# Kernel tuning notes

Hardware: AMD Instinct MI355X
Metric: run time of the kernel (lower is better)

## Reference

```python
import jax, jax.numpy as jnp
import numpy as np

B, N, NE = 16, 96, 256
ATOM, EDIM, HID, LAT, HEADS = 128, 16, 128, 128, 4
HD = LAT // HEADS
RBF, CUT, ZEMB, MAXZ = 16, 5.0, 32, 100
MUL0_IN, MUL1_IN = 64, 32      # irreps_node = 64x0e + 32x1o (dim 160)
MUL0_OUT, MUL1_OUT = 32, 16    # out irreps  = 32x0e + 16x1o (dim 80)
NODE_DIM = MUL0_IN + 3 * MUL1_IN
OUT_DIM = MUL0_OUT + 3 * MUL1_OUT
E_ATT = 1024
WNUM = MUL0_IN*MUL0_OUT + MUL0_IN*MUL1_OUT + MUL1_IN*MUL1_OUT + MUL1_IN*MUL0_OUT  # 4608


def _mlp3(x, w1, b1, w2, b2, w3, b3):
    x = jax.nn.silu(x @ w1 + b1)
    x = jax.nn.silu(x @ w2 + b2)
    return x @ w3 + b3


def setup_inputs() -> dict:
    key = jax.random.key(0)
    ks = jax.random.split(key, 40)
    s = 0.05  # scale params so deep MLP activations stay numerically sane
    d = {}
    d['h'] = jax.random.normal(ks[0], (B, N, ATOM), jnp.float32)
    d['h_full'] = jax.random.normal(ks[1], (B, N, NODE_DIM), jnp.float32)
    d['e_feat'] = jax.random.normal(ks[2], (NE, EDIM), jnp.float32)
    d['att_dist'] = jax.random.uniform(ks[3], (E_ATT,), jnp.float32)
    d['att_vec'] = jax.random.normal(ks[4], (E_ATT, 3), jnp.float32)
    d['z_emb_table'] = jax.random.normal(ks[5], (MAXZ + 1, ZEMB), jnp.float32) * s
    d['rw1'] = jax.random.normal(ks[6], (ZEMB + 1 + RBF, HID), jnp.float32) * s
    d['rb1'] = jnp.zeros((HID,), jnp.float32)
    d['rw2'] = jax.random.normal(ks[7], (HID, WNUM), jnp.float32) * s
    d['rb2'] = jnp.zeros((WNUM,), jnp.float32)
    d['ew1'] = jax.random.normal(ks[8], (EDIM, HID), jnp.float32) * s
    d['eb1'] = jnp.zeros((HID,), jnp.float32)
    d['ew2'] = jax.random.normal(ks[9], (HID, MUL0_OUT + MUL1_OUT), jnp.float32) * s
    d['eb2'] = jnp.zeros((MUL0_OUT + MUL1_OUT,), jnp.float32)
    d['qw1'] = jax.random.normal(ks[10], (ATOM + EDIM, HID), jnp.float32) * s
    d['qb1'] = jnp.zeros((HID,), jnp.float32)
    d['qw2'] = jax.random.normal(ks[11], (HID, HID), jnp.float32) * s
    d['qb2'] = jnp.zeros((HID,), jnp.float32)
    d['qw3'] = jax.random.normal(ks[12], (HID, LAT), jnp.float32) * s
    d['qb3'] = jnp.zeros((LAT,), jnp.float32)
    d['kw1'] = jax.random.normal(ks[13], (ATOM + ZEMB + 1 + RBF, HID), jnp.float32) * s
    d['kb1'] = jnp.zeros((HID,), jnp.float32)
    d['kw2'] = jax.random.normal(ks[14], (HID, HID), jnp.float32) * s
    d['kb2'] = jnp.zeros((HID,), jnp.float32)
    d['kw3'] = jax.random.normal(ks[15], (HID, LAT), jnp.float32) * s
    d['kb3'] = jnp.zeros((LAT,), jnp.float32)
    d['ow1'] = jax.random.normal(ks[16], (MUL0_OUT + MUL1_OUT, HID), jnp.float32) * s
    d['ob1'] = jnp.zeros((HID,), jnp.float32)
    d['ow2'] = jax.random.normal(ks[17], (HID, HID), jnp.float32) * s
    d['ob2'] = jnp.zeros((HID,), jnp.float32)
    d['ow3'] = jax.random.normal(ks[18], (HID, LAT), jnp.float32) * s
    d['ob3'] = jnp.zeros((LAT,), jnp.float32)
    d['z'] = jax.random.randint(ks[19], (B, N), 0, MAXZ)
    d['mask'] = jnp.ones((B, N), bool)
    d['absorber_index'] = jax.random.randint(ks[20], (B,), 0, N)
    d['att_dst'] = jnp.arange(E_ATT)  # unique flat indices into B*N
    return d


def reference(h, h_full, e_feat, att_dist, att_vec, z_emb_table,
              rw1, rb1, rw2, rb2, ew1, eb1, ew2, eb2,
              qw1, qb1, qw2, qb2, qw3, qb3,
              kw1, kb1, kw2, kb2, kw3, kb3,
              ow1, ob1, ow2, ob2, ow3, ob3,
              z, mask, absorber_index, att_dst):
    Bz, Na, Hd = h.shape
    F = Bz * Na
    nE = e_feat.shape[0]
    # scatter edge data into flat (B*N) atom slots
    am_flat = jnp.zeros((F,), bool).at[att_dst].set(True)
    d_flat = jnp.zeros((F,), h.dtype).at[att_dst].set(att_dist)
    v_flat = jnp.zeros((F, 3), h.dtype).at[att_dst].set(att_vec)
    att_mask = am_flat.reshape(Bz, Na) & mask
    # spherical harmonics (lmax=1, component normalization): Y0 = 1, Y1 = sqrt(3)*unit_vec
    un = v_flat / jnp.maximum(jnp.linalg.norm(v_flat, axis=-1, keepdims=True), 1e-8)
    y1 = jnp.sqrt(3.0) * un
    # Gaussian RBF on absorber->atom distance
    mu = jnp.linspace(0.0, CUT, RBF)
    delta = CUT / (RBF - 1)
    rbf = jnp.exp(-(d_flat[:, None] - mu) ** 2 / (2.0 * delta * delta))  # (F, RBF)
    zr = z_emb_table[z]                      # (B, N, ZEMB)
    zr_flat = zr.reshape(F, -1)
    is_abs = jnp.zeros((Bz, Na), h.dtype).at[jnp.arange(Bz), absorber_index].set(1.0)
    # radial MLP -> per-edge tensor-product weights
    w_in = jnp.concatenate([zr_flat, is_abs.reshape(F, 1), rbf], -1)
    tpw = jax.nn.silu(w_in @ rw1 + rb1) @ rw2 + rb2  # (F, WNUM)
    s1 = MUL0_IN * MUL0_OUT
    s2 = s1 + MUL0_IN * MUL1_OUT
    s3 = s2 + MUL1_IN * MUL1_OUT
    w00 = tpw[:, :s1].reshape(F, MUL0_IN, MUL0_OUT)   # 0e x 0e -> 0e
    w01 = tpw[:, s1:s2].reshape(F, MUL0_IN, MUL1_OUT) # 0e x 1o -> 1o
    w10 = tpw[:, s2:s3].reshape(F, MUL1_IN, MUL1_OUT) # 1o x 0e -> 1o
    w11 = tpw[:, s3:].reshape(F, MUL1_IN, MUL0_OUT)   # 1o x 1o -> 0e
    hf = h_full.reshape(F, -1)
    x0 = hf[:, :MUL0_IN]
    x1 = hf[:, MUL0_IN:].reshape(F, MUL1_IN, 3)
    alpha = 1.0 / jnp.sqrt(jnp.float32(MUL0_IN + MUL1_IN))  # path fan-in normalization
    c = 1.0 / jnp.sqrt(3.0)                                  # wigner-3j coeff for l=1 couplings
    out0 = alpha * (jnp.einsum('fi,fio->fo', x0, w00)
                    + c * jnp.einsum('fim,fm,fio->fo', x1, y1, w11))
    out1 = alpha * c * (jnp.einsum('fi,fm,fio->fom', x0, y1, w01)
                        + jnp.einsum('fim,fio->fom', x1, w10))
    v_irrep = jnp.concatenate([out0, out1.reshape(F, 3 * MUL1_OUT)], -1)  # (F, OUT_DIM)
    # cosine cutoff envelope + edge mask
    env = jnp.where(d_flat < CUT, 0.5 * (jnp.cos(jnp.pi * d_flat / CUT) + 1.0), 0.0)
    v_irrep = v_irrep * (am_flat.astype(h.dtype) * env)[:, None]
    # energy-conditioned per-irrep-channel modulation
    gates = jax.nn.silu(e_feat @ ew1 + eb1) @ ew2 + eb2  # (nE, 48)
    g_exp = jnp.concatenate([gates[:, :MUL0_OUT],
                             jnp.repeat(gates[:, MUL0_OUT:], 3, axis=-1)], -1)  # (nE, OUT_DIM)
    v_mod = (v_irrep[:, None, :] * g_exp[None]).reshape(Bz, Na, nE, OUT_DIM)
    # invariant multi-head scoring
    h_abs = h[jnp.arange(Bz), absorber_index]  # (B, H)
    q_in = jnp.concatenate([jnp.broadcast_to(h_abs[:, None], (Bz, nE, Hd)),
                            jnp.broadcast_to(e_feat[None], (Bz, nE, EDIM))], -1)
    q = _mlp3(q_in, qw1, qb1, qw2, qb2, qw3, qb3)  # (B, nE, LAT)
    atom_static = jnp.concatenate([h, zr, is_abs[..., None], rbf.reshape(Bz, Na, RBF)], -1)
    k = _mlp3(atom_static, kw1, kb1, kw2, kb2, kw3, kb3)  # (B, N, LAT)
    qh = q.reshape(Bz, nE, HEADS, HD)
    kh = k.reshape(Bz, Na, HEADS, HD)
    scores = (jnp.einsum('behd,bnhd->benh', qh, kh) * (HD ** -0.5)).mean(-1)  # (B, nE, N)
    m = att_mask[:, None, :]
    scores = jnp.where(m, scores, -1e9)
    attn = jax.nn.softmax(scores, axis=2) * m.astype(h.dtype)
    attn = attn / jnp.maximum(attn.sum(2, keepdims=True), 1e-8)
    out_irrep = jnp.einsum('ben,bnec->bec', attn, v_mod)  # (B, nE, OUT_DIM)
    # invariants: scalars + vector norms
    scal = out_irrep[..., :MUL0_OUT]
    vec = out_irrep[..., MUL0_OUT:].reshape(Bz, nE, MUL1_OUT, 3)
    inv = jnp.concatenate([scal, jnp.sqrt(jnp.sum(vec * vec, -1) + 1e-12)], -1)
    return _mlp3(inv, ow1, ob1, ow2, ob2, ow3, ob3)  # (B, nE, LAT)
```

## Files before the change

### kernel.cpp

```cpp
#include <hip/hip_runtime.h>
#include <hip/hip_fp16.h>
#include <math.h>

#define BB 16
#define NN 96
#define NE 256
#define FF (BB*NN)
#define ATOM 128
#define EDIM 16
#define HID 128
#define LAT 128
#define RBFN 16
#define CUTOFF 5.0f
#define ZEMB 32
#define E_ATT 1024
#define M0I 64
#define M1I 32
#define M0O 32
#define M1O 16
#define NODE_DIM 160
#define OUT_DIM 80
#define INVD 48
#define WNUM 4608
#define SEG1 2048
#define SEG2 3072
#define SEG3 3584

#define S1_EDGE 256
#define S1_Q    512
#define S1_GATE 16
#define S1_TRANS 144
#define STAGE1_BLKS 929

#define TP_BLKS 192
#define SCORE_BLKS 128
#define K2_BLKS (TP_BLKS + SCORE_BLKS)

#define CSTR 1544

typedef _Float16 half8_t __attribute__((ext_vector_type(8)));
typedef float float4v __attribute__((ext_vector_type(4)));

__device__ __forceinline__ float silu_f(float x) { return x / (1.0f + expf(-x)); }

__global__ __launch_bounds__(256) void k_stage1(
    const float* __restrict__ h, const float* __restrict__ z_emb, const int* __restrict__ z,
    const int* __restrict__ absorber, const float* __restrict__ e_feat,
    const int* __restrict__ att_dst, const float* __restrict__ att_dist,
    const float* __restrict__ att_vec,
    const float* __restrict__ rw1, const float* __restrict__ rb1,
    const float* __restrict__ kw1, const float* __restrict__ kb1,
    const float* __restrict__ kw2, const float* __restrict__ kb2,
    const float* __restrict__ kw3, const float* __restrict__ kb3,
    const float* __restrict__ qw1, const float* __restrict__ qb1,
    const float* __restrict__ qw2, const float* __restrict__ qb2,
    const float* __restrict__ qw3, const float* __restrict__ qb3,
    const float* __restrict__ ew1, const float* __restrict__ eb1,
    const float* __restrict__ ew2, const float* __restrict__ eb2,
    const float* __restrict__ rw2,
    __half* __restrict__ hiddenH, float* __restrict__ kmatw,
    float* __restrict__ qmat, float* __restrict__ gexp,
    __half* __restrict__ rw2T,
    int* __restrict__ inv, float* __restrict__ y1E, float* __restrict__ envE)
{
    __shared__ float smem[3488];
    int blk = blockIdx.x;
    int t = threadIdx.x;

    if (blk < S1_EDGE) {
        float (*sin1)[184] = (float(*)[184])smem;
        float (*l1S)[128]  = (float(*)[128])(smem + 736);
        float (*l2S)[128]  = (float(*)[128])(smem + 736 + 512);
        int w = t >> 6;
        int c = t & 63;
        int e = blk*4 + w;
        int f = att_dst[e];
        int b = f / NN, nn = f - b*NN;
        float d = att_dist[e];
        {
            float2 hv = *(const float2*)&h[f*ATOM + 2*c];
            sin1[w][2*c] = hv.x; sin1[w][2*c + 1] = hv.y;
        }
        if (c < ZEMB) sin1[w][ATOM + c] = z_emb[z[f]*ZEMB + c];
        if (c >= 32 && c < 48) {
            int j = c - 32;
            const float delta = CUTOFF / (RBFN - 1);
            float diff = d - j*delta;
            sin1[w][ATOM + ZEMB + 1 + j] = expf(-diff*diff / (2.0f*delta*delta));
        }
        if (c == 48) sin1[w][ATOM + ZEMB] = (absorber[b] == nn) ? 1.0f : 0.0f;
        __builtin_amdgcn_wave_barrier();
        int c2 = 2*c;
        {
            float2 a0 = *(const float2*)&rb1[c2];
            float2 a1 = make_float2(0.f, 0.f);
            #pragma unroll 8
            for (int i = 0; i < 48; i += 2) {
                float x0v = sin1[w][ATOM + i], x1v = sin1[w][ATOM + i + 1];
                float2 w0 = *(const float2*)&rw1[i*HID + c2];
                float2 w1 = *(const float2*)&rw1[(i+1)*HID + c2];
                a0.x += x0v*w0.x; a0.y += x0v*w0.y;
                a1.x += x1v*w1.x; a1.y += x1v*w1.y;
            }
            {
                float x0v = sin1[w][ATOM + 48];
                float2 w0 = *(const float2*)&rw1[48*HID + c2];
                a0.x += x0v*w0.x; a0.y += x0v*w0.y;
            }
            *(__half2*)&hiddenH[e*HID + c2] =
                __floats2half2_rn(silu_f(a0.x + a1.x), silu_f(a0.y + a1.y));
        }
        {
            float2 a0 = *(const float2*)&kb1[c2];
            float2 a1 = make_float2(0.f, 0.f);
            #pragma unroll 16
            for (int i = 0; i < 176; i += 2) {
                float x0v = sin1[w][i], x1v = sin1[w][i + 1];
                float2 w0 = *(const float2*)&kw1[i*HID + c2];
                float2 w1 = *(const float2*)&kw1[(i+1)*HID + c2];
                a0.x += x0v*w0.x; a0.y += x0v*w0.y;
                a1.x += x1v*w1.x; a1.y += x1v*w1.y;
            }
            {
                float x0v = sin1[w][176];
                float2 w0 = *(const float2*)&kw1[176*HID + c2];
                a0.x += x0v*w0.x; a0.y += x0v*w0.y;
            }
            l1S[w][c2] = silu_f(a0.x + a1.x); l1S[w][c2+1] = silu_f(a0.y + a1.y);
        }
        __builtin_amdgcn_wave_barrier();
        {
            float2 a0 = *(const float2*)&kb2[c2];
            float2 a1 = make_float2(0.f, 0.f);
            #pragma unroll 16
            for (int i = 0; i < HID; i += 2) {
                float x0v = l1S[w][i], x1v = l1S[w][i + 1];
                float2 w0 = *(const float2*)&kw2[i*HID + c2];
                float2 w1 = *(const float2*)&kw2[(i+1)*HID + c2];
                a0.x += x0v*w0.x; a0.y += x0v*w0.y;
                a1.x += x1v*w1.x; a1.y += x1v*w1.y;
            }
            l2S[w][c2] = silu_f(a0.x + a1.x); l2S[w][c2+1] = silu_f(a0.y + a1.y);
        }
        __builtin_amdgcn_wave_barrier();
        {
            float2 a0 = *(const float2*)&kb3[c2];
            float2 a1 = make_float2(0.f, 0.f);
            #pragma unroll 16
            for (int i = 0; i < HID; i += 2) {
                float x0v = l2S[w][i], x1v = l2S[w][i + 1];
                float2 w0 = *(const float2*)&kw3[i*HID + c2];
                float2 w1 = *(const float2*)&kw3[(i+1)*HID + c2];
                a0.x += x0v*w0.x; a0.y += x0v*w0.y;
                a1.x += x1v*w1.x; a1.y += x1v*w1.y;
            }
            float2 o; o.x = a0.x + a1.x; o.y = a0.y + a1.y;
            *(float2*)&kmatw[f*HID + c2] = o;
        }
    } else if (blk < S1_EDGE + S1_Q) {
        float* hA          = smem;
        float (*ef)[16]    = (float(*)[16])(smem + 128);
        float (*part)[128] = (float(*)[128])(smem + 256);
        float* l1S         = smem + 1280;
        float* l2S         = smem + 2304;
        int idx = blk - S1_EDGE;
        int r0 = idx * 8;
        int b  = r0 >> 8;
        int e8 = r0 & 255;
        if (t < 32) *(float4*)&hA[t*4] = *(const float4*)&h[(b*NN + absorber[b])*ATOM + t*4];
        if (t >= 128 && t < 256) { int e = (t - 128) >> 4, j = t & 15; ef[e][j] = e_feat[(e8 + e)*EDIM + j]; }
        __syncthreads();
        int r = t >> 5, c0 = (t & 31)*4;
        {
            float4 a0 = make_float4(0,0,0,0);
            int k0 = r*16;
            #pragma unroll
            for (int k = 0; k < 16; k++) {
                float hv = hA[k0 + k];
                float4 w0 = *(const float4*)&qw1[(k0 + k)*HID + c0];
                a0.x += hv*w0.x; a0.y += hv*w0.y; a0.z += hv*w0.z; a0.w += hv*w0.w;
            }
            *(float4*)&part[r][c0] = a0;
        }
        __syncthreads();
        {
            float4 s = *(const float4*)&qb1[c0];
            #pragma unroll
            for (int g = 0; g < 8; g++) {
                float4 pg = *(const float4*)&part[g][c0];
                s.x += pg.x; s.y += pg.y; s.z += pg.z; s.w += pg.w;
            }
            #pragma unroll
            for (int j = 0; j < 16; j++) {
                float a = ef[r][j];
                float4 w0 = *(const float4*)&qw1[(ATOM + j)*HID + c0];
                s.x += a*w0.x; s.y += a*w0.y; s.z += a*w0.z; s.w += a*w0.w;
            }
            l1S[r*128 + c0]   = silu_f(s.x); l1S[r*128 + c0+1] = silu_f(s.y);
            l1S[r*128 + c0+2] = silu_f(s.z); l1S[r*128 + c0+3] = silu_f(s.w);
        }
        __syncthreads();
        {
            float4 a0 = *(const float4*)&qb2[c0];
            float4 a1 = make_float4(0,0,0,0);
            #pragma unroll 8
            for (int i = 0; i < HID; i += 2) {
                float x0v = l1S[r*128 + i], x1v = l1S[r*128 + i+1];
                float4 w0 = *(const float4*)&qw2[i*HID + c0];
                float4 w1 = *(const float4*)&qw2[(i+1)*HID + c0];
                a0.x += x0v*w0.x; a0.y += x0v*w0.y; a0.z += x0v*w0.z; a0.w += x0v*w0.w;
                a1.x += x1v*w1.x; a1.y += x1v*w1.y; a1.z += x1v*w1.z; a1.w += x1v*w1.w;
            }
            l2S[r*128 + c0]   = silu_f(a0.x + a1.x); l2S[r*128 + c0+1] = silu_f(a0.y + a1.y);
            l2S[r*128 + c0+2] = silu_f(a0.z + a1.z); l2S[r*128 + c0+3] = silu_f(a0.w + a1.w);
        }
        __syncthreads();
        {
            float4 a0 = *(const float4*)&qb3[c0];
            float4 a1 = make_float4(0,0,0,0);
            #pragma unroll 8
            for (int i = 0; i < HID; i += 2) {
                float x0v = l2S[r*128 + i], x1v = l2S[r*128 + i+1];
                float4 w0 = *(const float4*)&qw3[i*HID + c0];
                float4 w1 = *(const float4*)&qw3[(i+1)*HID + c0];
                a0.x += x0v*w0.x; a0.y += x0v*w0.y; a0.z += x0v*w0.z; a0.w += x0v*w0.w;
                a1.x += x1v*w1.x; a1.y += x1v*w1.y; a1.z += x1v*w1.z; a1.w += x1v*w1.w;
            }
            float4 o;
            o.x = a0.x + a1.x; o.y = a0.y + a1.y; o.z = a0.z + a1.z; o.w = a0.w + a1.w;
            *(float4*)&qmat[(r0 + r)*LAT + c0] = o;
        }
    } else if (blk < S1_EDGE + S1_Q + S1_GATE) {
        float (*ef)[16]   = (float(*)[16])smem;
        float (*l1g)[128] = (float(*)[128])(smem + 256);
        float (*gg)[48]   = (float(*)[48])(smem + 256 + 2048);
        int e0 = (blk - S1_EDGE - S1_Q) * 16;
        { int e = t >> 4, i = t & 15; ef[e][i] = e_feat[(e0 + e)*EDIM + i]; }
        __syncthreads();
        int r = t >> 4, c0 = (t & 15)*8;
        {
            float4 a0 = *(const float4*)&eb1[c0];
            float4 a1 = *(const float4*)&eb1[c0 + 4];
            #pragma unroll
            for (int i = 0; i < EDIM; i++) {
                float a = ef[r][i];
                float4 w0 = *(const float4*)&ew1[i*HID + c0];
                float4 w1 = *(const float4*)&ew1[i*HID + c0 + 4];
                a0.x += a*w0.x; a0.y += a*w0.y; a0.z += a*w0.z; a0.w += a*w0.w;
                a1.x += a*w1.x; a1.y += a*w1.y; a1.z += a*w1.z; a1.w += a*w1.w;
            }
            l1g[r][c0]   = silu_f(a0.x); l1g[r][c0+1] = silu_f(a0.y);
            l1g[r][c0+2] = silu_f(a0.z); l1g[r][c0+3] = silu_f(a0.w);
            l1g[r][c0+4] = silu_f(a1.x); l1g[r][c0+5] = silu_f(a1.y);
            l1g[r][c0+6] = silu_f(a1.z); l1g[r][c0+7] = silu_f(a1.w);
        }
        __syncthreads();
        for (int u = t; u < 16*48; u += 256) {
            int e = u / 48, j = u - 48*(u/48);
            float acc = eb2[j];
            #pragma unroll 4
            for (int i = 0; i < HID; i++) acc += l1g[e][i]*ew2[i*48 + j];
            gg[e][j] = acc;
        }
        __syncthreads();
        for (int u = t; u < 16*80; u += 256) {
            int e = u / 80, cc = u - 80*(u/80);
            gexp[(e0 + e)*OUT_DIM + cc] = (cc < M0O) ? gg[e][cc] : gg[e][M0O + (cc - M0O)/3];
        }
    } else if (blk < S1_EDGE + S1_Q + S1_GATE + S1_TRANS) {
        __half* lds = (__half*)smem;
        int tb = blk - (S1_EDGE + S1_Q + S1_GATE);
        int nt = tb % 72, kt = tb / 72;
        int n0 = nt*64, k0 = kt*64;
        for (int p = 0; p < 16; p++) {
            int idx = t + 256*p;
            int kk = idx >> 6, nn = idx & 63;
            lds[nn*66 + kk] = __float2half(rw2[(k0+kk)*WNUM + n0+nn]);
        }
        __syncthreads();
        for (int p = 0; p < 16; p++) {
            int idx = t + 256*p;
            int nn = idx >> 6, kk = idx & 63;
            rw2T[(n0+nn)*HID + k0+kk] = lds[nn*66 + kk];
        }
    } else {
        for (int p = 0; p < 6; p++) inv[t + 256*p] = -1;
        for (int p = 0; p < 4; p++) {
            int e = t + 256*p;
            float d = att_dist[e];
            envE[e] = (d < CUTOFF) ? 0.5f*(cosf(3.14159265358979323846f*d/CUTOFF) + 1.0f) : 0.0f;
            float vx = att_vec[3*e], vy = att_vec[3*e+1], vz = att_vec[3*e+2];
            float nrm = sqrtf(vx*vx + vy*vy + vz*vz);
            float is = 1.0f / fmaxf(nrm, 1e-8f);
            const float s3 = 1.7320508075688772f;
            y1E[3*e]   = s3*vx*is;
            y1E[3*e+1] = s3*vy*is;
            y1E[3*e+2] = s3*vz*is;
        }
        __syncthreads();
        for (int p = 0; p < 4; p++) { int e = t + 256*p; inv[att_dst[e]] = e; }
    }
}

__global__ __launch_bounds__(256) void k_fuse(
    const __half* __restrict__ hiddenH, const __half* __restrict__ rw2T,
    const float* __restrict__ rb2,
    const float* __restrict__ qmat, const float* __restrict__ kmat,
    const int* __restrict__ inv, const int* __restrict__ att_dst,
    const float* __restrict__ h_full,
    const float* __restrict__ envE, const float* __restrict__ y1E,
    float* __restrict__ virr, float* __restrict__ scoresW)
{
    __shared__ __align__(16) char smemraw[62208];
    float* smem = (float*)smemraw;
    int blk = blockIdx.x;
    int t = threadIdx.x;
    if (blk < TP_BLKS) {
        __half* cS   = (__half*)smemraw;
        float* fbase = (float*)(smemraw + 49408);
        float* x0f   = fbase;
        float* x1f   = fbase + 1024;
        float* xyf   = fbase + 2560;
        float* y1f   = fbase + 3072;
        float* envf  = fbase + 3136;
        int*   fI    = (int*)(fbase + 3152);
        int cls  = blk % 3;
        int tile = blk / 3;
        int e0 = tile * 16;
        if (t < 16) {
            int e = e0 + t;
            fI[t] = att_dst[e];
            envf[t] = envE[e];
            y1f[t*4]   = y1E[3*e];
            y1f[t*4+1] = y1E[3*e+1];
            y1f[t*4+2] = y1E[3*e+2];
        }
        __syncthreads();
        for (int p = 0; p < 10; p++) {
            int idx = t + 256*p;
            int edge = idx / 160, j = idx - 160*edge;
            float v = h_full[fI[edge]*NODE_DIM + j];
            if (j < M0I) x0f[edge*64 + j] = v;
            else         x1f[edge*96 + (j - M0I)] = v;
        }
        __syncthreads();
        for (int p = 0; p < 2; p++) {
            int idx = t + 256*p;
            int edge = idx >> 5, i = idx & 31;
            xyf[edge*32 + i] = x1f[edge*96 + 3*i]*y1f[edge*4]
                             + x1f[edge*96 + 3*i+1]*y1f[edge*4+1]
                             + x1f[edge*96 + 3*i+2]*y1f[edge*4+2];
        }

        int wv = t >> 6;
        int lane = t & 63;
        int mrow = lane & 15, quad = lane >> 4;
        const _Float16* hp = (const _Float16*)hiddenH + (e0 + mrow)*HID + quad*8;
        half8_t af[4];
        #pragma unroll
        for (int kc = 0; kc < 4; kc++) af[kc] = *(const half8_t*)(hp + kc*32);

        int clsAdd = (cls == 1) ? 1 : 0;
        #pragma unroll 4
        for (int jj = 0; jj < 24; jj++) {
            int j = wv*24 + jj;
            int ntg = (cls == 2) ? (128 + j)
                                 : (2*j + clsAdd + ((j >= 64) ? 96 : 0));
            const _Float16* bp = (const _Float16*)rw2T + (ntg*16 + mrow)*HID + quad*8;
            float4v acc = {0.f, 0.f, 0.f, 0.f};
            #pragma unroll
            for (int kc = 0; kc < 4; kc++) {
                half8_t bf = *(const half8_t*)(bp + kc*32);
                acc = __builtin_amdgcn_mfma_f32_16x16x32_f16(af[kc], bf, acc, 0, 0, 0);
            }
            float bias = rb2[ntg*16 + mrow];
            #pragma unroll
            for (int r = 0; r < 4; r++)
                cS[(quad*4 + r)*CSTR + j*16 + mrow] = __float2half(acc[r] + bias);
        }
        __syncthreads();

        int edge = t >> 4, o = t & 15;
        const __half* cRow = cS + edge*CSTR + o;
        const float alpha = 0.10206207261596575f;
        const float ccf   = 0.5773502691896258f;
        int f = fI[edge];
        float env = envf[edge];
        if (cls < 2) {
            float t00 = 0.f, t11 = 0.f;
            #pragma unroll 8
            for (int j = 0; j < 64; j++)
                t00 += x0f[edge*64 + j]*__half2float(cRow[j*16]);
            #pragma unroll 8
            for (int j = 64; j < 96; j++)
                t11 += xyf[edge*32 + (j - 64)]*__half2float(cRow[j*16]);
            virr[f*OUT_DIM + cls*16 + o] = alpha*(t00 + ccf*t11)*env;
        } else {
            float t01 = 0.f, tm0 = 0.f, tm1 = 0.f, tm2 = 0.f;
            #pragma unroll 8
            for (int j = 0; j < 64; j++)
                t01 += x0f[edge*64 + j]*__half2float(cRow[j*16]);
            #pragma unroll 8
            for (int j = 64; j < 96; j++) {
                int i = j - 64;
                float C = __half2float(cRow[j*16]);
                tm0 += x1f[edge*96 + 3*i]*C;
                tm1 += x1f[edge*96 + 3*i+1]*C;
                tm2 += x1f[edge*96 + 3*i+2]*C;
            }
            float y0 = y1f[edge*4], y1v = y1f[edge*4+1], y2 = y1f[edge*4+2];
            virr[f*OUT_DIM + M0O + 3*o]     = alpha*ccf*(t01*y0 + tm0)*env;
            virr[f*OUT_DIM + M0O + 3*o + 1] = alpha*ccf*(t01*y1v + tm1)*env;
            virr[f*OUT_DIM + M0O + 3*o + 2] = alpha*ccf*(t01*y2 + tm2)*env;
        }
    } else {
        int u = blk - TP_BLKS;
        int b  = u >> 3;
        int e0 = (u & 7) * 32;
        float (*Qs)[132] = (float(*)[132])smem;
        float (*Kt)[132] = (float(*)[132])(smem + 32*132);
        float* mS = smem + 2*32*132;
        for (int p = 0; p < 4; p++) {
            int idx = t + 256*p; int e = idx >> 5, i4 = idx & 31;
            *(float4*)&Qs[e][i4*4] = *(const float4*)&qmat[(b*NE + e0 + e)*LAT + i4*4];
        }
        if (t < NN) mS[t] = ((unsigned)inv[b*NN + t] < E_ATT) ? 1.0f : 0.0f;
        int te = t >> 5, tn = t & 31;
        float acc[4][3] = {};
        for (int nt = 0; nt < 3; nt++) {
            __syncthreads();
            for (int p = 0; p < 4; p++) {
                int idx = t + 256*p; int n = idx >> 5, i4 = idx & 31;
                *(float4*)&Kt[n][i4*4] = *(const float4*)&kmat[(b*NN + nt*32 + n)*LAT + i4*4];
            }
            __syncthreads();
            for (int i = 0; i < LAT; i++) {
                float bv = Kt[tn][i];
                acc[0][nt] += Qs[te*4 + 0][i]*bv;
                acc[1][nt] += Qs[te*4 + 1][i]*bv;
                acc[2][nt] += Qs[te*4 + 2][i]*bv;
                acc[3][nt] += Qs[te*4 + 3][i]*bv;
            }
        }
        const float scale = 0.04419417382415922f;
        #pragma unroll
        for (int j = 0; j < 4; j++)
            #pragma unroll
            for (int jj = 0; jj < 3; jj++) {
                int n = tn + 32*jj;
                float s = (mS[n] != 0.f) ? acc[j][jj]*scale : -1e9f;
                scoresW[((b*NE) + e0 + te*4 + j)*NN + n] = s;
            }
    }
}

__global__ __launch_bounds__(256) void k_attf(
    const float* __restrict__ scoresW, const int* __restrict__ inv,
    const float* __restrict__ virr, const float* __restrict__ gexp,
    const float* __restrict__ ow1, const float* __restrict__ ob1,
    const float* __restrict__ ow2, const float* __restrict__ ob2,
    const float* __restrict__ ow3, const float* __restrict__ ob3,
    float* __restrict__ out)
{
    int b  = blockIdx.x >> 5;
    int e0 = (blockIdx.x & 31) * 8;
    int t = threadIdx.x;
    __shared__ float aS[8][100];
    __shared__ float gS[8][84];
    __shared__ float ocS[8][84];
    __shared__ float mS[NN];
    __shared__ float inS[8][INVD];
    __shared__ float l1S[8][HID];
    __shared__ float l2S[8][HID];

    for (int p = 0; p < 3; p++) {
        int idx = t + 256*p;
        int el = idx / NN, n = idx - NN*(idx/NN);
        aS[el][n] = scoresW[((b*NE) + e0 + el)*NN + n];
    }
    if (t < 160) {
        int el = t / 20, c4 = t - 20*(t/20);
        *(float4*)&gS[el][c4*4] = *(const float4*)&gexp[(e0 + el)*OUT_DIM + c4*4];
    }
    if (t < NN) mS[t] = ((unsigned)inv[b*NN + t] < E_ATT) ? 1.0f : 0.0f;
    __syncthreads();

    {
        int el = t >> 5;
        int ng = t & 31;
        float s0 = aS[el][ng], s1 = aS[el][ng + 32], s2 = aS[el][ng + 64];
        float m0 = mS[ng], m1 = mS[ng + 32], m2 = mS[ng + 64];
        float mx = fmaxf(s0, fmaxf(s1, s2));
        #pragma unroll
        for (int off = 1; off < 32; off <<= 1) mx = fmaxf(mx, __shfl_xor(mx, off));
        float e0v = expf(s0 - mx), e1v = expf(s1 - mx), e2v = expf(s2 - mx);
        float sm = e0v + e1v + e2v;
        #pragma unroll
        for (int off = 1; off < 32; off <<= 1) sm += __shfl_xor(sm, off);
        float r = 1.0f / sm;
        float p0 = m0*e0v*r, p1 = m1*e1v*r, p2 = m2*e2v*r;
        float ss = p0 + p1 + p2;
        #pragma unroll
        for (int off = 1; off < 32; off <<= 1) ss += __shfl_xor(ss, off);
        float is = 1.0f / fmaxf(ss, 1e-8f);
        aS[el][ng]      = p0*is;
        aS[el][ng + 32] = p1*is;
        aS[el][ng + 64] = p2*is;
    }
    __syncthreads();

    if (t < 160) {
        int el = t / 20, c4 = t - 20*(t/20);
        const float* vp = virr + (long)b*NN*OUT_DIM + c4*4;
        float4 acc = make_float4(0,0,0,0);
        #pragma unroll 4
        for (int n = 0; n < NN; n++) {
            float a = aS[el][n];
            float4 v = *(const float4*)&vp[n*OUT_DIM];
            acc.x += a*v.x; acc.y += a*v.y; acc.z += a*v.z; acc.w += a*v.w;
        }
        float4 g = *(float4*)&gS[el][c4*4];
        float4 o; o.x = acc.x*g.x; o.y = acc.y*g.y; o.z = acc.z*g.z; o.w = acc.w*g.w;
        *(float4*)&ocS[el][c4*4] = o;
    }
    __syncthreads();

    for (int u = t; u < 8*INVD; u += 256) {
        int el = u / INVD, j = u - INVD*(u/INVD);
        float val;
        if (j < M0O) val = ocS[el][j];
        else {
            int o = j - M0O;
            float x = ocS[el][M0O + 3*o], y = ocS[el][M0O + 3*o + 1], zz = ocS[el][M0O + 3*o + 2];
            val = sqrtf(x*x + y*y + zz*zz + 1e-12f);
        }
        inS[el][j] = val;
    }
    __syncthreads();

    int r = t >> 5, c0 = (t & 31)*4;
    {
        float4 a0 = *(const float4*)&ob1[c0];
        float4 a1 = make_float4(0,0,0,0);
        #pragma unroll 8
        for (int i = 0; i < INVD; i += 2) {
            float x0v = inS[r][i], x1v = inS[r][i+1];
            float4 w0 = *(const float4*)&ow1[i*HID + c0];
            float4 w1 = *(const float4*)&ow1[(i+1)*HID + c0];
            a0.x += x0v*w0.x; a0.y += x0v*w0.y; a0.z += x0v*w0.z; a0.w += x0v*w0.w;
            a1.x += x1v*w1.x; a1.y += x1v*w1.y; a1.z += x1v*w1.z; a1.w += x1v*w1.w;
        }
        l1S[r][c0]   = silu_f(a0.x + a1.x); l1S[r][c0+1] = silu_f(a0.y + a1.y);
        l1S[r][c0+2] = silu_f(a0.z + a1.z); l1S[r][c0+3] = silu_f(a0.w + a1.w);
    }
    __syncthreads();
    {
        float4 a0 = *(const float4*)&ob2[c0];
        float4 a1 = make_float4(0,0,0,0);
        #pragma unroll 8
        for (int i = 0; i < HID; i += 2) {
            float x0v = l1S[r][i], x1v = l1S[r][i+1];
            float4 w0 = *(const float4*)&ow2[i*HID + c0];
            float4 w1 = *(const float4*)&ow2[(i+1)*HID + c0];
            a0.x += x0v*w0.x; a0.y += x0v*w0.y; a0.z += x0v*w0.z; a0.w += x0v*w0.w;
            a1.x += x1v*w1.x; a1.y += x1v*w1.y; a1.z += x1v*w1.z; a1.w += x1v*w1.w;
        }
        l2S[r][c0]   = silu_f(a0.x + a1.x); l2S[r][c0+1] = silu_f(a0.y + a1.y);
        l2S[r][c0+2] = silu_f(a0.z + a1.z); l2S[r][c0+3] = silu_f(a0.w + a1.w);
    }
// ... 13 lines not shown
        o.x = a0.x + a1.x; o.y = a0.y + a1.y; o.z = a0.z + a1.z; o.w = a0.w + a1.w;
        *(float4*)&out[((b*NE + e0) + r)*LAT + c0] = o;
    }
}

extern "C" void kernel_launch(void* const* d_in, const int* in_sizes, int n_in,
                              void* d_out, int out_size, void* d_ws, size_t ws_size,
                              hipStream_t stream) {
    const float* h        = (const float*)d_in[0];
    const float* h_full   = (const float*)d_in[1];
    const float* e_feat   = (const float*)d_in[2];
    const float* att_dist = (const float*)d_in[3];
    const float* att_vec  = (const float*)d_in[4];
    const float* z_emb    = (const float*)d_in[5];
    const float* rw1 = (const float*)d_in[6];  const float* rb1 = (const float*)d_in[7];
    const float* rw2 = (const float*)d_in[8];  const float* rb2 = (const float*)d_in[9];
    const float* ew1 = (const float*)d_in[10]; const float* eb1 = (const float*)d_in[11];
    const float* ew2 = (const float*)d_in[12]; const float* eb2 = (const float*)d_in[13];
    const float* qw1 = (const float*)d_in[14]; const float* qb1 = (const float*)d_in[15];
    const float* qw2 = (const float*)d_in[16]; const float* qb2 = (const float*)d_in[17];
    const float* qw3 = (const float*)d_in[18]; const float* qb3 = (const float*)d_in[19];
    const float* kw1 = (const float*)d_in[20]; const float* kb1 = (const float*)d_in[21];
    const float* kw2 = (const float*)d_in[22]; const float* kb2 = (const float*)d_in[23];
    const float* kw3 = (const float*)d_in[24]; const float* kb3 = (const float*)d_in[25];
    const float* ow1 = (const float*)d_in[26]; const float* ob1 = (const float*)d_in[27];
    const float* ow2 = (const float*)d_in[28]; const float* ob2 = (const float*)d_in[29];
    const float* ow3 = (const float*)d_in[30]; const float* ob3 = (const float*)d_in[31];
    const int* z        = (const int*)d_in[32];
    const int* absorber = (const int*)d_in[34];
    const int* att_dst  = (const int*)d_in[35];

    float* ws = (float*)d_ws;
    int*   inv     = (int*)ws;
    float* y1E     = ws + 1536;
    float* envE    = ws + 4608;
    float* kmat    = ws + 5632;
    float* qmat    = ws + 202240;
    float* gexp    = ws + 726528;
    float* virr    = ws + 747008;
    float* scoresW = ws + 904704;
    __half* rw2T   = (__half*)(ws + 3657216);
    __half* hiddenH= (__half*)(ws + 3952128);

    float* out = (float*)d_out;

    k_stage1<<<STAGE1_BLKS, 256, 0, stream>>>(h, z_emb, z, absorber, e_feat,
                                              att_dst, att_dist, att_vec,
                                              rw1, rb1, kw1, kb1, kw2, kb2, kw3, kb3,
                                              qw1, qb1, qw2, qb2, qw3, qb3,
                                              ew1, eb1, ew2, eb2, rw2,
                                              hiddenH, kmat, qmat, gexp, rw2T,
                                              inv, y1E, envE);
    k_fuse<<<K2_BLKS, 256, 0, stream>>>(hiddenH, rw2T, rb2, qmat, kmat, inv,
                                        att_dst, h_full, envE, y1E, virr, scoresW);
    k_attf<<<BB*32, 256, 0, stream>>>(scoresW, inv, virr, gexp,
                                      ow1, ob1, ow2, ob2, ow3, ob3, out);
}
```

Before: 226.4 us.

## Merge stages into two kernels, fusing tensor product and scores into neighbors

Removes the middle kernel. The tensor-product blocks now compute the radial hidden layer, envelope and spherical harmonics in place and read rw2 directly, converting it to fp16 per element instead of using a pre-transposed copy. The attention scores move into the final kernel, which recomputes q·k per block instead of reading a scores buffer from global memory. This saves a launch and the intermediate buffers. In exchange, rw2 is loaded with strided, uncoalesced reads, and the edge-MLP blocks switch from wave barriers to full block barriers.

```diff
diff --git a/kernel.cpp b/kernel.cpp
--- a/kernel.cpp
+++ b/kernel.cpp
@@ -22,33 +22,29 @@
 #define OUT_DIM 80
 #define INVD 48
 #define WNUM 4608
-#define SEG1 2048
-#define SEG2 3072
-#define SEG3 3584
-
-#define S1_EDGE 256
-#define S1_Q    512
-#define S1_GATE 16
-#define S1_TRANS 144
-#define STAGE1_BLKS 929
-
-#define TP_BLKS 192
-#define SCORE_BLKS 128
-#define K2_BLKS (TP_BLKS + SCORE_BLKS)
-
-#define CSTR 1544
+
+#define K1_TP 192
+#define K1_EDGE_AT 192
+#define K1_Q_AT 448
+#define K1_GATE_AT 960
+#define K1_PREP_AT 976
+#define K1_BLKS 977
+
+#define CSTR2 520
 
 typedef _Float16 half8_t __attribute__((ext_vector_type(8)));
 typedef float float4v __attribute__((ext_vector_type(4)));
 
 __device__ __forceinline__ float silu_f(float x) { return x / (1.0f + expf(-x)); }
 
-__global__ __launch_bounds__(256) void k_stage1(
-    const float* __restrict__ h, const float* __restrict__ z_emb, const int* __restrict__ z,
+__global__ __launch_bounds__(256) void k1(
+    const float* __restrict__ h, const float* __restrict__ h_full,
+    const float* __restrict__ z_emb, const int* __restrict__ z,
     const int* __restrict__ absorber, const float* __restrict__ e_feat,
     const int* __restrict__ att_dst, const float* __restrict__ att_dist,
     const float* __restrict__ att_vec,
     const float* __restrict__ rw1, const float* __restrict__ rb1,
+    const float* __restrict__ rw2, const float* __restrict__ rb2,
     const float* __restrict__ kw1, const float* __restrict__ kb1,
     const float* __restrict__ kw2, const float* __restrict__ kb2,
     const float* __restrict__ kw3, const float* __restrict__ kb3,
@@ -57,23 +53,186 @@
     const float* __restrict__ qw3, const float* __restrict__ qb3,
     const float* __restrict__ ew1, const float* __restrict__ eb1,
     const float* __restrict__ ew2, const float* __restrict__ eb2,
-    const float* __restrict__ rw2,
-    __half* __restrict__ hiddenH, float* __restrict__ kmatw,
-    float* __restrict__ qmat, float* __restrict__ gexp,
-    __half* __restrict__ rw2T,
-    int* __restrict__ inv, float* __restrict__ y1E, float* __restrict__ envE)
+    float* __restrict__ kmatw, float* __restrict__ qmat,
+    float* __restrict__ gexp, float* __restrict__ virr,
+    int* __restrict__ inv)
 {
-    __shared__ float smem[3488];
+    __shared__ __align__(16) char smemraw[36864];
+    float* smem = (float*)smemraw;
     int blk = blockIdx.x;
     int t = threadIdx.x;
 
-    if (blk < S1_EDGE) {
+    if (blk < K1_TP) {
+        __half* cS    = (__half*)smemraw;
+        float*  fbase = (float*)(smemraw + 16640);
+        float* x0f  = fbase;
+        float* x1f  = fbase + 1024;
+        float* xyf  = fbase + 2560;
+        float* y1f  = fbase + 3072;
+        float* envf = fbase + 3136;
+        float* dS   = fbase + 3152;
+        int*   fI   = (int*)(fbase + 3168);
+        float* winf = fbase + 3184;
+        _Float16* hS = (_Float16*)(smemraw + 32704);
+
+        int cls  = blk % 3;
+        int tile = blk / 3;
+        int e0t = tile * 16;
+        if (t < 16) {
+            int e = e0t + t;
+            int f = att_dst[e];
+            fI[t] = f;
+            float d = att_dist[e];
+            dS[t] = d;
+            envf[t] = (d < CUTOFF) ? 0.5f*(cosf(3.14159265358979323846f*d/CUTOFF) + 1.0f) : 0.0f;
+            float vx = att_vec[3*e], vy = att_vec[3*e+1], vz = att_vec[3*e+2];
+            float nrm = sqrtf(vx*vx + vy*vy + vz*vz);
+            float is = 1.0f / fmaxf(nrm, 1e-8f);
+            const float s3 = 1.7320508075688772f;
+            y1f[t*4]   = s3*vx*is;
+            y1f[t*4+1] = s3*vy*is;
+            y1f[t*4+2] = s3*vz*is;
+        }
+        __syncthreads();
+        for (int u = t; u < 16*49; u += 256) {
+            int e = u / 49, j = u - 49*(u/49);
+            int f = fI[e];
+            float v;
+            if (j < ZEMB) v = z_emb[z[f]*ZEMB + j];
+            else if (j == ZEMB) { int b = f / NN, nn = f - b*NN; v = (absorber[b] == nn) ? 1.0f : 0.0f; }
+            else {
+                int jr = j - 33;
+                const float delta = CUTOFF / (RBFN - 1);
+                float diff = dS[e] - jr*delta;
+                v = expf(-diff*diff / (2.0f*delta*delta));
+            }
+            winf[e*52 + j] = v;
+        }
+        for (int p = 0; p < 10; p++) {
+            int idx = t + 256*p;
+            int edge = idx / 160, j = idx - 160*edge;
+            float v = h_full[fI[edge]*NODE_DIM + j];
+            if (j < M0I) x0f[edge*64 + j] = v;
+            else         x1f[edge*96 + (j - M0I)] = v;
+        }
+        __syncthreads();
+        for (int p = 0; p < 2; p++) {
+            int idx = t + 256*p;
+            int edge = idx >> 5, i = idx & 31;
+            xyf[edge*32 + i] = x1f[edge*96 + 3*i]*y1f[edge*4]
+                             + x1f[edge*96 + 3*i+1]*y1f[edge*4+1]
+                             + x1f[edge*96 + 3*i+2]*y1f[edge*4+2];
+        }
+        {
+            int e = t >> 4;
+            const float* wf = winf + e*52;
+            #pragma unroll
+            for (int p = 0; p < 4; p++) {
+                int c2 = 2*((t & 15) + 16*p);
+                float2 a0 = *(const float2*)&rb1[c2];
+                float2 a1 = make_float2(0.f, 0.f);
+                #pragma unroll 8
+                for (int i = 0; i < 48; i += 2) {
+                    float x0v = wf[i], x1v = wf[i + 1];
+                    float2 w0 = *(const float2*)&rw1[i*HID + c2];
+                    float2 w1 = *(const float2*)&rw1[(i+1)*HID + c2];
+                    a0.x += x0v*w0.x; a0.y += x0v*w0.y;
+                    a1.x += x1v*w1.x; a1.y += x1v*w1.y;
+                }
+                {
+                    float x0v = wf[48];
+                    float2 w0 = *(const float2*)&rw1[48*HID + c2];
+                    a0.x += x0v*w0.x; a0.y += x0v*w0.y;
+                }
+                *(__half2*)&hS[e*128 + c2] =
+                    __floats2half2_rn(silu_f(a0.x + a1.x), silu_f(a0.y + a1.y));
+            }
+        }
+        __syncthreads();
+
+        int wv = t >> 6;
+        int lane = t & 63;
+        int mrow = lane & 15, quad = lane >> 4;
+        half8_t af[4];
+        #pragma unroll
+        for (int kc = 0; kc < 4; kc++)
+            af[kc] = *(const half8_t*)&hS[mrow*128 + quad*8 + kc*32];
+
+        int edge = t >> 4, o = t & 15;
+        float t00 = 0.f, t11 = 0.f;
+        float t01 = 0.f, tm0 = 0.f, tm1 = 0.f, tm2 = 0.f;
+        int clsAdd = (cls == 1) ? 1 : 0;
+
+        for (int g = 0; g < 3; g++) {
+            #pragma unroll
+            for (int jj = 0; jj < 8; jj++) {
+                int jl = wv*8 + jj;
+                int j = g*32 + jl;
+                int ntg = (cls == 2) ? (128 + j)
+                                     : (2*j + clsAdd + ((j >= 64) ? 96 : 0));
+                const float* bcol = rw2 + ntg*16 + mrow;
+                float4v acc = {0.f, 0.f, 0.f, 0.f};
+                #pragma unroll
+                for (int kc = 0; kc < 4; kc++) {
+                    half8_t bfr;
+                    #pragma unroll
+                    for (int m = 0; m < 8; m++)
+                        bfr[m] = (_Float16)bcol[(quad*8 + kc*32 + m)*WNUM];
+                    acc = __builtin_amdgcn_mfma_f32_16x16x32_f16(af[kc], bfr, acc, 0, 0, 0);
+                }
+                float bias = rb2[ntg*16 + mrow];
+                #pragma unroll
+                for (int r = 0; r < 4; r++)
+                    cS[(quad*4 + r)*CSTR2 + jl*16 + mrow] = __float2half(acc[r] + bias);
+            }
+            __syncthreads();
+            const __half* cRow = cS + edge*CSTR2 + o;
+            if (cls < 2) {
+                if (g < 2) {
+                    #pragma unroll 8
+                    for (int jl = 0; jl < 32; jl++)
+                        t00 += x0f[edge*64 + g*32 + jl]*__half2float(cRow[jl*16]);
+                } else {
+                    #pragma unroll 8
+                    for (int jl = 0; jl < 32; jl++)
+                        t11 += xyf[edge*32 + jl]*__half2float(cRow[jl*16]);
+                }
+            } else {
+                if (g < 2) {
+                    #pragma unroll 8
+                    for (int jl = 0; jl < 32; jl++)
+                        t01 += x0f[edge*64 + g*32 + jl]*__half2float(cRow[jl*16]);
+                } else {
+                    #pragma unroll 8
+                    for (int jl = 0; jl < 32; jl++) {
+                        float C = __half2float(cRow[jl*16]);
+                        tm0 += x1f[edge*96 + 3*jl]*C;
+                        tm1 += x1f[edge*96 + 3*jl+1]*C;
+                        tm2 += x1f[edge*96 + 3*jl+2]*C;
+                    }
+                }
+            }
+            __syncthreads();
+        }
+        const float alpha = 0.10206207261596575f;
+        const float ccf   = 0.5773502691896258f;
+        int f = fI[edge];
+        float env = envf[edge];
+        if (cls < 2) {
+            virr[f*OUT_DIM + cls*16 + o] = alpha*(t00 + ccf*t11)*env;
+        } else {
+            float y0 = y1f[edge*4], y1v = y1f[edge*4+1], y2 = y1f[edge*4+2];
+            virr[f*OUT_DIM + M0O + 3*o]     = alpha*ccf*(t01*y0 + tm0)*env;
+            virr[f*OUT_DIM + M0O + 3*o + 1] = alpha*ccf*(t01*y1v + tm1)*env;
+            virr[f*OUT_DIM + M0O + 3*o + 2] = alpha*ccf*(t01*y2 + tm2)*env;
+        }
+    } else if (blk < K1_Q_AT) {
         float (*sin1)[184] = (float(*)[184])smem;
         float (*l1S)[128]  = (float(*)[128])(smem + 736);
         float (*l2S)[128]  = (float(*)[128])(smem + 736 + 512);
         int w = t >> 6;
         int c = t & 63;
-        int e = blk*4 + w;
+        int e = (blk - K1_EDGE_AT)*4 + w;
         int f = att_dst[e];
         int b = f / NN, nn = f - b*NN;
         float d = att_dist[e];
@@ -89,31 +248,12 @@
             sin1[w][ATOM + ZEMB + 1 + j] = expf(-diff*diff / (2.0f*delta*delta));
         }
         if (c == 48) sin1[w][ATOM + ZEMB] = (absorber[b] == nn) ? 1.0f : 0.0f;
-        __builtin_amdgcn_wave_barrier();
+        __syncthreads();
         int c2 = 2*c;
         {
-            float2 a0 = *(const float2*)&rb1[c2];
+            float2 a0 = *(const float2*)&kb1[c2];
             float2 a1 = make_float2(0.f, 0.f);
             #pragma unroll 8
-            for (int i = 0; i < 48; i += 2) {
-                float x0v = sin1[w][ATOM + i], x1v = sin1[w][ATOM + i + 1];
-                float2 w0 = *(const float2*)&rw1[i*HID + c2];
-                float2 w1 = *(const float2*)&rw1[(i+1)*HID + c2];
-                a0.x += x0v*w0.x; a0.y += x0v*w0.y;
-                a1.x += x1v*w1.x; a1.y += x1v*w1.y;
-            }
-            {
-                float x0v = sin1[w][ATOM + 48];
-                float2 w0 = *(const float2*)&rw1[48*HID + c2];
-                a0.x += x0v*w0.x; a0.y += x0v*w0.y;
-            }
-            *(__half2*)&hiddenH[e*HID + c2] =
-                __floats2half2_rn(silu_f(a0.x + a1.x), silu_f(a0.y + a1.y));
-        }
-        {
-            float2 a0 = *(const float2*)&kb1[c2];
-            float2 a1 = make_float2(0.f, 0.f);
-            #pragma unroll 16
             for (int i = 0; i < 176; i += 2) {
                 float x0v = sin1[w][i], x1v = sin1[w][i + 1];
                 float2 w0 = *(const float2*)&kw1[i*HID + c2];
@@ -128,11 +268,11 @@
             }
             l1S[w][c2] = silu_f(a0.x + a1.x); l1S[w][c2+1] = silu_f(a0.y + a1.y);
         }
-        __builtin_amdgcn_wave_barrier();
+        __syncthreads();
         {
             float2 a0 = *(const float2*)&kb2[c2];
             float2 a1 = make_float2(0.f, 0.f);
-            #pragma unroll 16
+            #pragma unroll 8
             for (int i = 0; i < HID; i += 2) {
                 float x0v = l1S[w][i], x1v = l1S[w][i + 1];
                 float2 w0 = *(const float2*)&kw2[i*HID + c2];
@@ -142,11 +282,11 @@
             }
             l2S[w][c2] = silu_f(a0.x + a1.x); l2S[w][c2+1] = silu_f(a0.y + a1.y);
         }
-        __builtin_amdgcn_wave_barrier();
+        __syncthreads();
         {
             float2 a0 = *(const float2*)&kb3[c2];
             float2 a1 = make_float2(0.f, 0.f);
-            #pragma unroll 16
+            #pragma unroll 8
             for (int i = 0; i < HID; i += 2) {
                 float x0v = l2S[w][i], x1v = l2S[w][i + 1];
                 float2 w0 = *(const float2*)&kw3[i*HID + c2];
@@ -157,13 +297,13 @@
             float2 o; o.x = a0.x + a1.x; o.y = a0.y + a1.y;
             *(float2*)&kmatw[f*HID + c2] = o;
         }
-    } else if (blk < S1_EDGE + S1_Q) {
+    } else if (blk < K1_GATE_AT) {
         float* hA          = smem;
         float (*ef)[16]    = (float(*)[16])(smem + 128);
         float (*part)[128] = (float(*)[128])(smem + 256);
         float* l1S         = smem + 1280;
         float* l2S         = smem + 2304;
-        int idx = blk - S1_EDGE;
+        int idx = blk - K1_Q_AT;
         int r0 = idx * 8;
         int b  = r0 >> 8;
         int e8 = r0 & 255;
@@ -230,11 +370,11 @@
             o.x = a0.x + a1.x; o.y = a0.y + a1.y; o.z = a0.z + a1.z; o.w = a0.w + a1.w;
             *(float4*)&qmat[(r0 + r)*LAT + c0] = o;
         }
-    } else if (blk < S1_EDGE + S1_Q + S1_GATE) {
+    } else if (blk < K1_PREP_AT) {
         float (*ef)[16]   = (float(*)[16])smem;
         float (*l1g)[128] = (float(*)[128])(smem + 256);
         float (*gg)[48]   = (float(*)[48])(smem + 256 + 2048);
-        int e0 = (blk - S1_EDGE - S1_Q) * 16;
+        int e0 = (blk - K1_GATE_AT) * 16;
         { int e = t >> 4, i = t & 15; ef[e][i] = e_feat[(e0 + e)*EDIM + i]; }
         __syncthreads();
         int r = t >> 4, c0 = (t & 15)*8;
@@ -267,195 +407,16 @@
             int e = u / 80, cc = u - 80*(u/80);
             gexp[(e0 + e)*OUT_DIM + cc] = (cc < M0O) ? gg[e][cc] : gg[e][M0O + (cc - M0O)/3];
         }
-    } else if (blk < S1_EDGE + S1_Q + S1_GATE + S1_TRANS) {
-        __half* lds = (__half*)smem;
-        int tb = blk - (S1_EDGE + S1_Q + S1_GATE);
-        int nt = tb % 72, kt = tb / 72;
-        int n0 = nt*64, k0 = kt*64;
-        for (int p = 0; p < 16; p++) {
-            int idx = t + 256*p;
-            int kk = idx >> 6, nn = idx & 63;
-            lds[nn*66 + kk] = __float2half(rw2[(k0+kk)*WNUM + n0+nn]);
-        }
-        __syncthreads();
-        for (int p = 0; p < 16; p++) {
-            int idx = t + 256*p;
-            int nn = idx >> 6, kk = idx & 63;
-            rw2T[(n0+nn)*HID + k0+kk] = lds[nn*66 + kk];
-        }
     } else {
         for (int p = 0; p < 6; p++) inv[t + 256*p] = -1;
-        for (int p = 0; p < 4; p++) {
-            int e = t + 256*p;
-            float d = att_dist[e];
-            envE[e] = (d < CUTOFF) ? 0.5f*(cosf(3.14159265358979323846f*d/CUTOFF) + 1.0f) : 0.0f;
-            float vx = att_vec[3*e], vy = att_vec[3*e+1], vz = att_vec[3*e+2];
-            float nrm = sqrtf(vx*vx + vy*vy + vz*vz);
-            float is = 1.0f / fmaxf(nrm, 1e-8f);
-            const float s3 = 1.7320508075688772f;
-            y1E[3*e]   = s3*vx*is;
-            y1E[3*e+1] = s3*vy*is;
-            y1E[3*e+2] = s3*vz*is;
-        }
         __syncthreads();
         for (int p = 0; p < 4; p++) { int e = t + 256*p; inv[att_dst[e]] = e; }
     }
 }
 
-__global__ __launch_bounds__(256) void k_fuse(
-    const __half* __restrict__ hiddenH, const __half* __restrict__ rw2T,
-    const float* __restrict__ rb2,
+__global__ __launch_bounds__(256) void k_attf(
     const float* __restrict__ qmat, const float* __restrict__ kmat,
-    const int* __restrict__ inv, const int* __restrict__ att_dst,
-    const float* __restrict__ h_full,
-    const float* __restrict__ envE, const float* __restrict__ y1E,
-    float* __restrict__ virr, float* __restrict__ scoresW)
-{
-    __shared__ __align__(16) char smemraw[62208];
-    float* smem = (float*)smemraw;
-    int blk = blockIdx.x;
-    int t = threadIdx.x;
-    if (blk < TP_BLKS) {
-        __half* cS   = (__half*)smemraw;
-        float* fbase = (float*)(smemraw + 49408);
-        float* x0f   = fbase;
-        float* x1f   = fbase + 1024;
-        float* xyf   = fbase + 2560;
-        float* y1f   = fbase + 3072;
-        float* envf  = fbase + 3136;
-        int*   fI    = (int*)(fbase + 3152);
-        int cls  = blk % 3;
-        int tile = blk / 3;
-        int e0 = tile * 16;
-        if (t < 16) {
-            int e = e0 + t;
-            fI[t] = att_dst[e];
-            envf[t] = envE[e];
-            y1f[t*4]   = y1E[3*e];
-            y1f[t*4+1] = y1E[3*e+1];
-            y1f[t*4+2] = y1E[3*e+2];
-        }
-        __syncthreads();
-        for (int p = 0; p < 10; p++) {
-            int idx = t + 256*p;
-            int edge = idx / 160, j = idx - 160*edge;
-            float v = h_full[fI[edge]*NODE_DIM + j];
-            if (j < M0I) x0f[edge*64 + j] = v;
-            else         x1f[edge*96 + (j - M0I)] = v;
-        }
-        __syncthreads();
-        for (int p = 0; p < 2; p++) {
-            int idx = t + 256*p;
-            int edge = idx >> 5, i = idx & 31;
-            xyf[edge*32 + i] = x1f[edge*96 + 3*i]*y1f[edge*4]
-                             + x1f[edge*96 + 3*i+1]*y1f[edge*4+1]
-                             + x1f[edge*96 + 3*i+2]*y1f[edge*4+2];
-        }
-
-        int wv = t >> 6;
-        int lane = t & 63;
-        int mrow = lane & 15, quad = lane >> 4;
-        const _Float16* hp = (const _Float16*)hiddenH + (e0 + mrow)*HID + quad*8;
-        half8_t af[4];
-        #pragma unroll
-        for (int kc = 0; kc < 4; kc++) af[kc] = *(const half8_t*)(hp + kc*32);
-
-        int clsAdd = (cls == 1) ? 1 : 0;
-        #pragma unroll 4
-        for (int jj = 0; jj < 24; jj++) {
-            int j = wv*24 + jj;
-            int ntg = (cls == 2) ? (128 + j)
-                                 : (2*j + clsAdd + ((j >= 64) ? 96 : 0));
-            const _Float16* bp = (const _Float16*)rw2T + (ntg*16 + mrow)*HID + quad*8;
-            float4v acc = {0.f, 0.f, 0.f, 0.f};
-            #pragma unroll
-            for (int kc = 0; kc < 4; kc++) {
-                half8_t bf = *(const half8_t*)(bp + kc*32);
-                acc = __builtin_amdgcn_mfma_f32_16x16x32_f16(af[kc], bf, acc, 0, 0, 0);
-            }
-            float bias = rb2[ntg*16 + mrow];
-            #pragma unroll
-            for (int r = 0; r < 4; r++)
-                cS[(quad*4 + r)*CSTR + j*16 + mrow] = __float2half(acc[r] + bias);
-        }
-        __syncthreads();
-
-        int edge = t >> 4, o = t & 15;
-        const __half* cRow = cS + edge*CSTR + o;
-        const float alpha = 0.10206207261596575f;
-        const float ccf   = 0.5773502691896258f;
-        int f = fI[edge];
-        float env = envf[edge];
-        if (cls < 2) {
-            float t00 = 0.f, t11 = 0.f;
-            #pragma unroll 8
-            for (int j = 0; j < 64; j++)
-                t00 += x0f[edge*64 + j]*__half2float(cRow[j*16]);
-            #pragma unroll 8
-            for (int j = 64; j < 96; j++)
-                t11 += xyf[edge*32 + (j - 64)]*__half2float(cRow[j*16]);
-            virr[f*OUT_DIM + cls*16 + o] = alpha*(t00 + ccf*t11)*env;
-        } else {
-            float t01 = 0.f, tm0 = 0.f, tm1 = 0.f, tm2 = 0.f;
-            #pragma unroll 8
-            for (int j = 0; j < 64; j++)
-                t01 += x0f[edge*64 + j]*__half2float(cRow[j*16]);
-            #pragma unroll 8
-            for (int j = 64; j < 96; j++) {
-                int i = j - 64;
-                float C = __half2float(cRow[j*16]);
-                tm0 += x1f[edge*96 + 3*i]*C;
-                tm1 += x1f[edge*96 + 3*i+1]*C;
-                tm2 += x1f[edge*96 + 3*i+2]*C;
-            }
-            float y0 = y1f[edge*4], y1v = y1f[edge*4+1], y2 = y1f[edge*4+2];
-            virr[f*OUT_DIM + M0O + 3*o]     = alpha*ccf*(t01*y0 + tm0)*env;
-            virr[f*OUT_DIM + M0O + 3*o + 1] = alpha*ccf*(t01*y1v + tm1)*env;
-            virr[f*OUT_DIM + M0O + 3*o + 2] = alpha*ccf*(t01*y2 + tm2)*env;
-        }
-    } else {
-        int u = blk - TP_BLKS;
-        int b  = u >> 3;
-        int e0 = (u & 7) * 32;
-        float (*Qs)[132] = (float(*)[132])smem;
-        float (*Kt)[132] = (float(*)[132])(smem + 32*132);
-        float* mS = smem + 2*32*132;
-        for (int p = 0; p < 4; p++) {
-            int idx = t + 256*p; int e = idx >> 5, i4 = idx & 31;
-            *(float4*)&Qs[e][i4*4] = *(const float4*)&qmat[(b*NE + e0 + e)*LAT + i4*4];
-        }
-        if (t < NN) mS[t] = ((unsigned)inv[b*NN + t] < E_ATT) ? 1.0f : 0.0f;
-        int te = t >> 5, tn = t & 31;
-        float acc[4][3] = {};
-        for (int nt = 0; nt < 3; nt++) {
-            __syncthreads();
-            for (int p = 0; p < 4; p++) {
-                int idx = t + 256*p; int n = idx >> 5, i4 = idx & 31;
-                *(float4*)&Kt[n][i4*4] = *(const float4*)&kmat[(b*NN + nt*32 + n)*LAT + i4*4];
-            }
-            __syncthreads();
-            for (int i = 0; i < LAT; i++) {
-                float bv = Kt[tn][i];
-                acc[0][nt] += Qs[te*4 + 0][i]*bv;
-                acc[1][nt] += Qs[te*4 + 1][i]*bv;
-                acc[2][nt] += Qs[te*4 + 2][i]*bv;
-                acc[3][nt] += Qs[te*4 + 3][i]*bv;
-            }
-        }
-        const float scale = 0.04419417382415922f;
-        #pragma unroll
-        for (int j = 0; j < 4; j++)
-            #pragma unroll
-            for (int jj = 0; jj < 3; jj++) {
-                int n = tn + 32*jj;
-                float s = (mS[n] != 0.f) ? acc[j][jj]*scale : -1e9f;
-                scoresW[((b*NE) + e0 + te*4 + j)*NN + n] = s;
-            }
-    }
-}
-
-__global__ __launch_bounds__(256) void k_attf(
-    const float* __restrict__ scoresW, const int* __restrict__ inv,
+    const int* __restrict__ inv,
     const float* __restrict__ virr, const float* __restrict__ gexp,
     const float* __restrict__ ow1, const float* __restrict__ ob1,
     const float* __restrict__ ow2, const float* __restrict__ ob2,
@@ -465,31 +426,49 @@
     int b  = blockIdx.x >> 5;
     int e0 = (blockIdx.x & 31) * 8;
     int t = threadIdx.x;
-    __shared__ float aS[8][100];
-    __shared__ float gS[8][84];
-    __shared__ float ocS[8][84];
-    __shared__ float mS[NN];
-    __shared__ float inS[8][INVD];
-    __shared__ float l1S[8][HID];
-    __shared__ float l2S[8][HID];
-
-    for (int p = 0; p < 3; p++) {
-        int idx = t + 256*p;
-        int el = idx / NN, n = idx - NN*(idx/NN);
-        aS[el][n] = scoresW[((b*NE) + e0 + el)*NN + n];
-    }
+    __shared__ float smem[7936];
+    float (*aS)[100]   = (float(*)[100])smem;
+    float (*gS)[84]    = (float(*)[84])(smem + 800);
+    float (*ocS)[84]   = (float(*)[84])(smem + 1472);
+    float* mS          = smem + 2144;
+    float (*inS)[INVD] = (float(*)[INVD])(smem + 2240);
+    float (*q8)[132]   = (float(*)[132])(smem + 2624);
+    float* Kt          = smem + 3680;
+    float (*l1S)[HID]  = (float(*)[HID])(smem + 3680);
+    float (*l2S)[HID]  = (float(*)[HID])(smem + 3680 + 1024);
+
     if (t < 160) {
         int el = t / 20, c4 = t - 20*(t/20);
         *(float4*)&gS[el][c4*4] = *(const float4*)&gexp[(e0 + el)*OUT_DIM + c4*4];
     }
     if (t < NN) mS[t] = ((unsigned)inv[b*NN + t] < E_ATT) ? 1.0f : 0.0f;
-    __syncthreads();
-
     {
-        int el = t >> 5;
-        int ng = t & 31;
-        float s0 = aS[el][ng], s1 = aS[el][ng + 32], s2 = aS[el][ng + 64];
+        int el = t >> 5, i4 = t & 31;
+        *(float4*)&q8[el][i4*4] = *(const float4*)&qmat[(b*NE + e0 + el)*LAT + i4*4];
+    }
+
+    int el = t >> 5, tn = t & 31;
+    float sacc0 = 0.f, sacc1 = 0.f, sacc2 = 0.f;
+    #pragma unroll
+    for (int nt = 0; nt < 3; nt++) {
+        __syncthreads();
+        for (int p = 0; p < 4; p++) {
+            int idx = t + 256*p; int n = idx >> 5, i4 = idx & 31;
+            *(float4*)&Kt[n*133 + i4*4] = *(const float4*)&kmat[(b*NN + nt*32 + n)*LAT + i4*4];
+        }
+        __syncthreads();
+        float acc = 0.f;
+        for (int i = 0; i < LAT; i++) acc += q8[el][i]*Kt[tn*133 + i];
+        if (nt == 0) sacc0 = acc; else if (nt == 1) sacc1 = acc; else sacc2 = acc;
+    }
+
+    {
+        const float scale = 0.04419417382415922f;
+        int ng = tn;
         float m0 = mS[ng], m1 = mS[ng + 32], m2 = mS[ng + 64];
+        float s0 = (m0 != 0.f) ? sacc0*scale : -1e9f;
+        float s1 = (m1 != 0.f) ? sacc1*scale : -1e9f;
+        float s2 = (m2 != 0.f) ? sacc2*scale : -1e9f;
         float mx = fmaxf(s0, fmaxf(s1, s2));
         #pragma unroll
         for (int off = 1; off < 32; off <<= 1) mx = fmaxf(mx, __shfl_xor(mx, off));
@@ -510,31 +489,31 @@
     __syncthreads();
 
     if (t < 160) {
-        int el = t / 20, c4 = t - 20*(t/20);
+        int el2 = t / 20, c4 = t - 20*(t/20);
         const float* vp = virr + (long)b*NN*OUT_DIM + c4*4;
         float4 acc = make_float4(0,0,0,0);
         #pragma unroll 4
         for (int n = 0; n < NN; n++) {
-            float a = aS[el][n];
+            float a = aS[el2][n];
             float4 v = *(const float4*)&vp[n*OUT_DIM];
             acc.x += a*v.x; acc.y += a*v.y; acc.z += a*v.z; acc.w += a*v.w;
         }
-        float4 g = *(float4*)&gS[el][c4*4];
+        float4 g = *(float4*)&gS[el2][c4*4];
         float4 o; o.x = acc.x*g.x; o.y = acc.y*g.y; o.z = acc.z*g.z; o.w = acc.w*g.w;
-        *(float4*)&ocS[el][c4*4] = o;
+        *(float4*)&ocS[el2][c4*4] = o;
     }
     __syncthreads();
 
     for (int u = t; u < 8*INVD; u += 256) {
-        int el = u / INVD, j = u - INVD*(u/INVD);
+        int el2 = u / INVD, j = u - INVD*(u/INVD);
         float val;
-        if (j < M0O) val = ocS[el][j];
+        if (j < M0O) val = ocS[el2][j];
         else {
             int o = j - M0O;
-            float x = ocS[el][M0O + 3*o], y = ocS[el][M0O + 3*o + 1], zz = ocS[el][M0O + 3*o + 2];
+            float x = ocS[el2][M0O + 3*o], y = ocS[el2][M0O + 3*o + 1], zz = ocS[el2][M0O + 3*o + 2];
             val = sqrtf(x*x + y*y + zz*zz + 1e-12f);
         }
-        inS[el][j] = val;
+        inS[el2][j] = val;
     }
     __syncthreads();
 
@@ -614,27 +593,20 @@
 
     float* ws = (float*)d_ws;
     int*   inv     = (int*)ws;
-    float* y1E     = ws + 1536;
-    float* envE    = ws + 4608;
     float* kmat    = ws + 5632;
     float* qmat    = ws + 202240;
     float* gexp    = ws + 726528;
     float* virr    = ws + 747008;
-    float* scoresW = ws + 904704;
-    __half* rw2T   = (__half*)(ws + 3657216);
-    __half* hiddenH= (__half*)(ws + 3952128);
 
     float* out = (float*)d_out;
 
-    k_stage1<<<STAGE1_BLKS, 256, 0, stream>>>(h, z_emb, z, absorber, e_feat,
-                                              att_dst, att_dist, att_vec,
-                                              rw1, rb1, kw1, kb1, kw2, kb2, kw3, kb3,
-                                              qw1, qb1, qw2, qb2, qw3, qb3,
-                                              ew1, eb1, ew2, eb2, rw2,
-                                              hiddenH, kmat, qmat, gexp, rw2T,
-                                              inv, y1E, envE);
-    k_fuse<<<K2_BLKS, 256, 0, stream>>>(hiddenH, rw2T, rb2, qmat, kmat, inv,
-                                        att_dst, h_full, envE, y1E, virr, scoresW);
-    k_attf<<<BB*32, 256, 0, stream>>>(scoresW, inv, virr, gexp,
+    k1<<<K1_BLKS, 256, 0, stream>>>(h, h_full, z_emb, z, absorber, e_feat,
+                                    att_dst, att_dist, att_vec,
+                                    rw1, rb1, rw2, rb2,
+                                    kw1, kb1, kw2, kb2, kw3, kb3,
+                                    qw1, qb1, qw2, qb2, qw3, qb3,
+                                    ew1, eb1, ew2, eb2,
+                                    kmat, qmat, gexp, virr, inv);
+    k_attf<<<BB*32, 256, 0, stream>>>(qmat, kmat, inv, virr, gexp,
                                       ow1, ob1, ow2, ob2, ow3, ob3, out);
 }
```

Measured after the change: 211.4 us. 1.07x faster.
